# Kernel tuning notes

Measured on AMD Instinct MI355X. Metric: run time of the kernel, lower is better.

## Reference

```python
import jax, jax.numpy as jnp
import numpy as np

B, N, D, MAX_ATOMS, K = 1024, 50000, 256, 200, 8


def setup_inputs() -> dict:
    key = jax.random.key(0)
    k1, k2, k3, k4 = jax.random.split(key, 4)
    return {
        "query_embedding": jax.random.normal(k1, (B, D), dtype=jnp.float32),
        "memory_embeddings": jax.random.normal(k2, (N, D), dtype=jnp.float32),
        "memory_som_masks": jax.random.uniform(k3, (N, MAX_ATOMS), dtype=jnp.float32),
        "W": jax.random.normal(k4, (D, D), dtype=jnp.float32) / jnp.sqrt(jnp.float32(D)),
        "b": jnp.zeros((D,), dtype=jnp.float32),
        "k": K,
    }


def _to_poincare(x, W, b):
    # Linear + Tanh, then rescale into the Poincare ball (radius <= 0.95)
    h = jnp.tanh(x @ W + b)
    norm = jnp.linalg.norm(h, axis=-1, keepdims=True)
    scale = jnp.where(norm > 0.95, 0.95 / norm, jnp.ones_like(norm))
    return h * scale


def _hyperbolic_distance(x, y):
    # ||x_i - y_j||^2 via expansion (same math as broadcasted diff, no [B,N,D] blowup)
    x_sq = jnp.sum(x * x, axis=-1, keepdims=True)            # [B,1]
    y_sq = jnp.sum(y * y, axis=-1)[None, :]                   # [1,N]
    diff_sq = jnp.maximum(x_sq + y_sq - 2.0 * (x @ y.T), 0.0)  # [B,N]
    denom = (1.0 - x_sq) * (1.0 - y_sq)
    arg = 1.0 + 2.0 * diff_sq / (denom + 1e-8)
    return jnp.arccosh(jnp.maximum(arg, 1.0 + 1e-6))


def reference(query_embedding, memory_embeddings, memory_som_masks, W, b, k):
    query_hyp = _to_poincare(query_embedding, W, b)
    memory_hyp = _to_poincare(memory_embeddings, W, b)
    dists = _hyperbolic_distance(query_hyp, memory_hyp)       # [B,N]
    # smallest-k distances
    neg_top, top_idx = jax.lax.top_k(-dists, k)               # [B,k]
    top_dists = -neg_top
    weights = jax.nn.softmax(-top_dists, axis=-1)             # [B,k]
    som_hints = memory_som_masks[top_idx]                     # [B,k,MAX_ATOMS]
    return weights, som_hints
```

## Files before the change

### kernel.cpp

```cpp
#include <hip/hip_runtime.h>
#include <hip/hip_bf16.h>
#include <math.h>
#include <float.h>

#define B_Q   1024
#define N_M   50000
#define DIM   256
#define ATOMS 200
#define KSEL  8
#define NCHUNK 40
#define CHUNK  1250
#define MT    128
#define NMT   10
#define CPC   8
#define NC    (NCHUNK * CPC)
#define T16   16
#define TROWS 64
#define APX   264

typedef __attribute__((ext_vector_type(8))) short bf16x8;
typedef __attribute__((ext_vector_type(4))) float f32x4;

static __device__ inline unsigned short f2bf(float f) {
  __hip_bfloat16 h = __float2bfloat16(f);
  return *reinterpret_cast<unsigned short*>(&h);
}

static __device__ inline void split3(float x, unsigned short& s1,
                                     unsigned short& s2, unsigned short& s3) {
  __hip_bfloat16 b1 = __float2bfloat16(x);
  float f1 = __bfloat162float(b1);
  float r1 = x - f1;
  __hip_bfloat16 b2 = __float2bfloat16(r1);
  float f2 = __bfloat162float(b2);
  __hip_bfloat16 b3 = __float2bfloat16(r1 - f2);
  s1 = *reinterpret_cast<unsigned short*>(&b1);
  s2 = *reinterpret_cast<unsigned short*>(&b2);
  s3 = *reinterpret_cast<unsigned short*>(&b3);
}

static __device__ inline void split3t(float x, unsigned short& s1,
                                      unsigned short& s2, unsigned short& s3) {
  const unsigned u = __float_as_uint(x);
  s1 = (unsigned short)(u >> 16);
  const float f1 = __uint_as_float(u & 0xffff0000u);
  const float r1 = x - f1;
  const unsigned v = __float_as_uint(r1);
  s2 = (unsigned short)(v >> 16);
  const float f2 = __uint_as_float(v & 0xffff0000u);
  const float r2 = r1 - f2;
  s3 = (unsigned short)(__float_as_uint(r2) >> 16);
}

static __device__ inline float tanh32(float z) {
  float tz = fabsf(z) * 2.885390082f;
  tz = fminf(tz, 120.f);
  const float E = __builtin_amdgcn_exp2f(tz);
  const float T = 1.f - 2.f / (E + 1.f);
  return (z >= 0.f) ? T : -T;
}

__global__ __launch_bounds__(256) void wsplit_kernel(
    const float* __restrict__ W,
    unsigned short* __restrict__ Wt1, unsigned short* __restrict__ Wt2,
    unsigned short* __restrict__ Wt3)
{
  const int n = blockIdx.x;
  const int k = threadIdx.x;
  unsigned short s1, s2, s3;
  split3(W[(size_t)k * DIM + n], s1, s2, s3);
  Wt1[(size_t)n * DIM + k] = s1;
  Wt2[(size_t)n * DIM + k] = s2;
  Wt3[(size_t)n * DIM + k] = s3;
}

__global__ __launch_bounds__(1024) void transform_kernel(
    const float* __restrict__ X, int nrows,
    const unsigned short* __restrict__ Wt1, const unsigned short* __restrict__ Wt2,
    const unsigned short* __restrict__ Wt3, const float* __restrict__ bvec,
    float* __restrict__ H, unsigned short* __restrict__ Hb,
    float2* __restrict__ aux)
{
  __shared__ __align__(16) unsigned short X1s[TROWS * APX];
  __shared__ __align__(16) unsigned short X2s[TROWS * APX];
  __shared__ __align__(16) unsigned short X3s[TROWS * APX];
  __shared__ float red[16][TROWS];
  __shared__ float sArr[TROWS];

  const int t    = threadIdx.x;
  const int lane = t & 63;
  const int wave = t >> 6;
  const int row0 = blockIdx.x * TROWS;

  {
    const int r  = t >> 4;
    const int c0 = (t & 15) * 16;
    int gr = row0 + r; if (gr >= nrows) gr = nrows - 1;
    const float4* src = (const float4*)(X + (size_t)gr * DIM + c0);
    bf16x8 p1[2], p2[2], p3[2];
#pragma unroll
    for (int half = 0; half < 2; ++half) {
#pragma unroll
      for (int v = 0; v < 2; ++v) {
        const float4 x4 = src[half * 2 + v];
        const float xv[4] = {x4.x, x4.y, x4.z, x4.w};
#pragma unroll
        for (int i = 0; i < 4; ++i) {
          unsigned short s1, s2, s3;
          split3t(xv[i], s1, s2, s3);
          p1[half][v * 4 + i] = (short)s1;
          p2[half][v * 4 + i] = (short)s2;
          p3[half][v * 4 + i] = (short)s3;
        }
      }
      *(bf16x8*)(X1s + r * APX + c0 + half * 8) = p1[half];
      *(bf16x8*)(X2s + r * APX + c0 + half * 8) = p2[half];
      *(bf16x8*)(X3s + r * APX + c0 + half * 8) = p3[half];
    }
  }
  __syncthreads();

  const int lx   = lane & 15;
  const int quad = lane >> 4;
  const int n0   = wave * 16;

  f32x4 acc[4];
#pragma unroll
  for (int ms = 0; ms < 4; ++ms) { acc[ms][0] = 0.f; acc[ms][1] = 0.f; acc[ms][2] = 0.f; acc[ms][3] = 0.f; }

  const size_t brow = (size_t)(n0 + lx) * DIM + quad * 8;
  bf16x8 b1c = *(const bf16x8*)(Wt1 + brow);
  bf16x8 b2c = *(const bf16x8*)(Wt2 + brow);
  bf16x8 b3c = *(const bf16x8*)(Wt3 + brow);

#pragma unroll
  for (int ks = 0; ks < 8; ++ks) {
    bf16x8 b1n, b2n, b3n;
    if (ks < 7) {
      const size_t nb = brow + (ks + 1) * 32;
      b1n = *(const bf16x8*)(Wt1 + nb);
      b2n = *(const bf16x8*)(Wt2 + nb);
      b3n = *(const bf16x8*)(Wt3 + nb);
    }
    const int ko = ks * 32 + quad * 8;
#pragma unroll
    for (int ms = 0; ms < 4; ++ms) {
      const int ar = (ms * 16 + lx) * APX + ko;
      const bf16x8 a1 = *(const bf16x8*)(X1s + ar);
      const bf16x8 a2 = *(const bf16x8*)(X2s + ar);
      const bf16x8 a3 = *(const bf16x8*)(X3s + ar);
      acc[ms] = __builtin_amdgcn_mfma_f32_16x16x32_bf16(a1, b1c, acc[ms], 0, 0, 0);
      acc[ms] = __builtin_amdgcn_mfma_f32_16x16x32_bf16(a1, b2c, acc[ms], 0, 0, 0);
      acc[ms] = __builtin_amdgcn_mfma_f32_16x16x32_bf16(a2, b1c, acc[ms], 0, 0, 0);
      acc[ms] = __builtin_amdgcn_mfma_f32_16x16x32_bf16(a1, b3c, acc[ms], 0, 0, 0);
      acc[ms] = __builtin_amdgcn_mfma_f32_16x16x32_bf16(a2, b2c, acc[ms], 0, 0, 0);
      acc[ms] = __builtin_amdgcn_mfma_f32_16x16x32_bf16(a3, b1c, acc[ms], 0, 0, 0);
    }
    b1c = b1n; b2c = b2n; b3c = b3n;
  }

  const float bb = bvec[n0 + lx];
  float h[4][4];
#pragma unroll
  for (int ms = 0; ms < 4; ++ms)
#pragma unroll
    for (int r = 0; r < 4; ++r)
      h[ms][r] = tanh32(acc[ms][r] + bb);

  float p[4][4];
#pragma unroll
  for (int ms = 0; ms < 4; ++ms)
#pragma unroll
    for (int r = 0; r < 4; ++r) p[ms][r] = h[ms][r] * h[ms][r];
#pragma unroll
  for (int off = 1; off < 16; off <<= 1)
#pragma unroll
    for (int ms = 0; ms < 4; ++ms)
#pragma unroll
      for (int r = 0; r < 4; ++r) p[ms][r] += __shfl_xor(p[ms][r], off);
  if (lx == 0)
#pragma unroll
    for (int ms = 0; ms < 4; ++ms)
#pragma unroll
      for (int r = 0; r < 4; ++r) red[wave][ms * 16 + quad * 4 + r] = p[ms][r];
  __syncthreads();

  if (t < TROWS) {
    float nsq = 0.f;
#pragma unroll
    for (int w = 0; w < 16; ++w) nsq += red[w][t];
    const float nrm = sqrtf(nsq);
    sArr[t] = (nrm > 0.95f) ? (0.95f / nrm) : 1.f;
  }
  __syncthreads();

  float u[4][4];
#pragma unroll
  for (int ms = 0; ms < 4; ++ms)
#pragma unroll
    for (int r = 0; r < 4; ++r) {
      const float sc = sArr[ms * 16 + quad * 4 + r];
      u[ms][r] = h[ms][r] * sc;
      p[ms][r] = u[ms][r] * u[ms][r];
    }
#pragma unroll
  for (int off = 1; off < 16; off <<= 1)
#pragma unroll
    for (int ms = 0; ms < 4; ++ms)
#pragma unroll
      for (int r = 0; r < 4; ++r) p[ms][r] += __shfl_xor(p[ms][r], off);
  if (lx == 0)
#pragma unroll
    for (int ms = 0; ms < 4; ++ms)
#pragma unroll
      for (int r = 0; r < 4; ++r) red[wave][ms * 16 + quad * 4 + r] = p[ms][r];

#pragma unroll
  for (int ms = 0; ms < 4; ++ms)
#pragma unroll
    for (int r = 0; r < 4; ++r) {
      const int grow = row0 + ms * 16 + quad * 4 + r;
      if (grow < nrows) {
        H[(size_t)grow * DIM + n0 + lx]  = u[ms][r];
        Hb[(size_t)grow * DIM + n0 + lx] = f2bf(u[ms][r]);
      }
    }
  __syncthreads();
  if (t < TROWS) {
    const int grow = row0 + t;
    if (grow < nrows) {
      float ysq = 0.f;
#pragma unroll
      for (int w = 0; w < 16; ++w) ysq += red[w][t];
      aux[grow] = make_float2(ysq, 1.f / (1.f - ysq));
    }
  }
}

__global__ __launch_bounds__(256) void score_kernel(
    const unsigned short* __restrict__ Hqb, const unsigned short* __restrict__ Hmb,
    const float2* __restrict__ auxq, const float2* __restrict__ auxm,
    float* __restrict__ cand_s, int* __restrict__ cand_i)
{
  __shared__ __align__(16) unsigned short Afs[16 * 64 * 8];
  __shared__ unsigned long long wtop[4][32][CPC];

  const int t    = threadIdx.x;
  const int lane = t & 63;
  const int wave = t >> 6;
  const int q0   = blockIdx.y * 32;
  const int c    = blockIdx.x;
  const int mbase = c * CHUNK;
  const int lx   = lane & 15;
  const int quad = lane >> 4;

#pragma unroll
  for (int i = 0; i < 4; ++i) {
    const int sl = wave * 4 + i;
    const int ks = sl >> 1, qs = sl & 1;
    const bf16x8 a = *(const bf16x8*)(Hqb + (size_t)(q0 + qs * 16 + lx) * DIM + ks * 32 + quad * 8);
    *(bf16x8*)(Afs + ((size_t)sl * 64 + lane) * 8) = a;
  }
  const float xq0 = auxq[q0 +      quad * 4 + 0].x;
  const float xq1 = auxq[q0 +      quad * 4 + 1].x;
  const float xq2 = auxq[q0 +      quad * 4 + 2].x;
  const float xq3 = auxq[q0 +      quad * 4 + 3].x;
  const float xq4 = auxq[q0 + 16 + quad * 4 + 0].x;
  const float xq5 = auxq[q0 + 16 + quad * 4 + 1].x;
  const float xq6 = auxq[q0 + 16 + quad * 4 + 2].x;
  const float xq7 = auxq[q0 + 16 + quad * 4 + 3].x;
  __syncthreads();

  unsigned long long t0a=~0ULL,t0b=~0ULL,t0c=~0ULL, t1a=~0ULL,t1b=~0ULL,t1c=~0ULL;
  unsigned long long t2a=~0ULL,t2b=~0ULL,t2c=~0ULL, t3a=~0ULL,t3b=~0ULL,t3c=~0ULL;
  unsigned long long t4a=~0ULL,t4b=~0ULL,t4c=~0ULL, t5a=~0ULL,t5b=~0ULL,t5c=~0ULL;
  unsigned long long t6a=~0ULL,t6b=~0ULL,t6c=~0ULL, t7a=~0ULL,t7b=~0ULL,t7c=~0ULL;

  const int colw = wave * 32 + lx;
  int midx = mbase + colw;

  const unsigned short* B0p = Hmb + (size_t)midx * DIM + quad * 8;
  const unsigned short* B1p = B0p + (size_t)16 * DIM;

#define KSTEP(KS, BA, BB) do {                                                        \
    const bf16x8 a0_ = *(const bf16x8*)(Afs + (((KS) * 2 + 0) * 64 + lane) * 8);      \
    const bf16x8 a1_ = *(const bf16x8*)(Afs + (((KS) * 2 + 1) * 64 + lane) * 8);      \
    acc00 = __builtin_amdgcn_mfma_f32_16x16x32_bf16(a0_, BA, acc00, 0, 0, 0);         \
    acc01 = __builtin_amdgcn_mfma_f32_16x16x32_bf16(a0_, BB, acc01, 0, 0, 0);         \
    acc10 = __builtin_amdgcn_mfma_f32_16x16x32_bf16(a1_, BA, acc10, 0, 0, 0);         \
    acc11 = __builtin_amdgcn_mfma_f32_16x16x32_bf16(a1_, BB, acc11, 0, 0, 0);         \
  } while (0)

#define SCOREU(ACC, R, YM, RO, GI, XQ, T0, T1, T2) do {                               \
    const float sv_ = fmaxf(fmaf(-2.f, (ACC)[R], (XQ) + (YM)), 0.f) * (RO);           \
    const unsigned long long pk_ =                                                     \
      (((unsigned long long)__float_as_uint(sv_)) << 32) | (unsigned int)(GI);         \
    if (pk_ < T2) {                                                                    \
      T2 = pk_;                                                                        \
      if (T2 < T1) { const unsigned long long x_ = T1; T1 = T2; T2 = x_; }             \
      if (T1 < T0) { const unsigned long long x_ = T0; T0 = T1; T1 = x_; }             \
    }                                                                                  \
  } while (0)

#define SCOREM(ACC, R, YM, RO, OK, GI, XQ, T0, T1, T2) do {                           \
    const float sv_ = fmaxf(fmaf(-2.f, (ACC)[R], (XQ) + (YM)), 0.f) * (RO);           \
    const unsigned long long pk_ =                                                     \
      (((unsigned long long)__float_as_uint(sv_)) << 32) | (unsigned int)(GI);         \
    if ((OK) && pk_ < T2) {                                                            \
      T2 = pk_;                                                                        \
      if (T2 < T1) { const unsigned long long x_ = T1; T1 = T2; T2 = x_; }             \
      if (T1 < T0) { const unsigned long long x_ = T0; T0 = T1; T1 = x_; }             \
    }                                                                                  \
  } while (0)

#define SCORE16U do {                                                                 \
    const float ym0 = aux0.x, ro0 = aux0.y;                                           \
    const float ym1 = aux1.x, ro1 = aux1.y;                                           \
    const int   gi0 = midx;                                                           \
    const int   gi1 = midx + 16;                                                      \
    SCOREU(acc00, 0, ym0, ro0, gi0, xq0, t0a, t0b, t0c);                              \
    SCOREU(acc00, 1, ym0, ro0, gi0, xq1, t1a, t1b, t1c);                              \
    SCOREU(acc00, 2, ym0, ro0, gi0, xq2, t2a, t2b, t2c);                              \
    SCOREU(acc00, 3, ym0, ro0, gi0, xq3, t3a, t3b, t3c);                              \
    SCOREU(acc01, 0, ym1, ro1, gi1, xq0, t0a, t0b, t0c);                              \
    SCOREU(acc01, 1, ym1, ro1, gi1, xq1, t1a, t1b, t1c);                              \
    SCOREU(acc01, 2, ym1, ro1, gi1, xq2, t2a, t2b, t2c);                              \
    SCOREU(acc01, 3, ym1, ro1, gi1, xq3, t3a, t3b, t3c);                              \
    SCOREU(acc10, 0, ym0, ro0, gi0, xq4, t4a, t4b, t4c);                              \
    SCOREU(acc10, 1, ym0, ro0, gi0, xq5, t5a, t5b, t5c);                              \
    SCOREU(acc10, 2, ym0, ro0, gi0, xq6, t6a, t6b, t6c);                              \
    SCOREU(acc10, 3, ym0, ro0, gi0, xq7, t7a, t7b, t7c);                              \
    SCOREU(acc11, 0, ym1, ro1, gi1, xq4, t4a, t4b, t4c);                              \
    SCOREU(acc11, 1, ym1, ro1, gi1, xq5, t5a, t5b, t5c);                              \
    SCOREU(acc11, 2, ym1, ro1, gi1, xq6, t6a, t6b, t6c);                              \
    SCOREU(acc11, 3, ym1, ro1, gi1, xq7, t7a, t7b, t7c);                              \
  } while (0)

#define SCORE16M(OK0, OK1) do {                                                       \
    const float ym0 = aux0.x, ro0 = aux0.y;                                           \
    const float ym1 = aux1.x, ro1 = aux1.y;                                           \
    const int   gi0 = midx;                                                           \
    const int   gi1 = midx + 16;                                                      \
    SCOREM(acc00, 0, ym0, ro0, OK0, gi0, xq0, t0a, t0b, t0c);                         \
    SCOREM(acc00, 1, ym0, ro0, OK0, gi0, xq1, t1a, t1b, t1c);                         \
    SCOREM(acc00, 2, ym0, ro0, OK0, gi0, xq2, t2a, t2b, t2c);                         \
    SCOREM(acc00, 3, ym0, ro0, OK0, gi0, xq3, t3a, t3b, t3c);                         \
    SCOREM(acc01, 0, ym1, ro1, OK1, gi1, xq0, t0a, t0b, t0c);                         \
    SCOREM(acc01, 1, ym1, ro1, OK1, gi1, xq1, t1a, t1b, t1c);                         \
    SCOREM(acc01, 2, ym1, ro1, OK1, gi1, xq2, t2a, t2b, t2c);                         \
    SCOREM(acc01, 3, ym1, ro1, OK1, gi1, xq3, t3a, t3b, t3c);                         \
    SCOREM(acc10, 0, ym0, ro0, OK0, gi0, xq4, t4a, t4b, t4c);                         \
    SCOREM(acc10, 1, ym0, ro0, OK0, gi0, xq5, t5a, t5b, t5c);                         \
    SCOREM(acc10, 2, ym0, ro0, OK0, gi0, xq6, t6a, t6b, t6c);                         \
    SCOREM(acc10, 3, ym0, ro0, OK0, gi0, xq7, t7a, t7b, t7c);                         \
    SCOREM(acc11, 0, ym1, ro1, OK1, gi1, xq4, t4a, t4b, t4c);                         \
    SCOREM(acc11, 1, ym1, ro1, OK1, gi1, xq5, t5a, t5b, t5c);                         \
    SCOREM(acc11, 2, ym1, ro1, OK1, gi1, xq6, t6a, t6b, t6c);                         \
    SCOREM(acc11, 3, ym1, ro1, OK1, gi1, xq7, t7a, t7b, t7c);                         \
  } while (0)

  bf16x8 xA0 = *(const bf16x8*)(B0p + 0);
  bf16x8 xA1 = *(const bf16x8*)(B0p + 32);
  bf16x8 xA2 = *(const bf16x8*)(B0p + 64);
  bf16x8 xA3 = *(const bf16x8*)(B0p + 96);
  bf16x8 xB0 = *(const bf16x8*)(B1p + 0);
  bf16x8 xB1 = *(const bf16x8*)(B1p + 32);
  bf16x8 xB2 = *(const bf16x8*)(B1p + 64);
  bf16x8 xB3 = *(const bf16x8*)(B1p + 96);

  for (int mt = 0; mt < NMT - 1; ++mt) {
    bf16x8 yA0 = *(const bf16x8*)(B0p + 128);
    bf16x8 yA1 = *(const bf16x8*)(B0p + 160);
    bf16x8 yA2 = *(const bf16x8*)(B0p + 192);
    bf16x8 yA3 = *(const bf16x8*)(B0p + 224);
    bf16x8 yB0 = *(const bf16x8*)(B1p + 128);
    bf16x8 yB1 = *(const bf16x8*)(B1p + 160);
    bf16x8 yB2 = *(const bf16x8*)(B1p + 192);
    bf16x8 yB3 = *(const bf16x8*)(B1p + 224);
    const float2 aux0 = auxm[midx];
    const float2 aux1 = auxm[midx + 16];

    f32x4 acc00 = {0.f, 0.f, 0.f, 0.f};
    f32x4 acc01 = {0.f, 0.f, 0.f, 0.f};
    f32x4 acc10 = {0.f, 0.f, 0.f, 0.f};
    f32x4 acc11 = {0.f, 0.f, 0.f, 0.f};

    KSTEP(0, xA0, xB0);
    KSTEP(1, xA1, xB1);
    KSTEP(2, xA2, xB2);
    KSTEP(3, xA3, xB3);

    B0p += (size_t)MT * DIM;
    B1p += (size_t)MT * DIM;
    xA0 = *(const bf16x8*)(B0p + 0);
    xA1 = *(const bf16x8*)(B0p + 32);
    xA2 = *(const bf16x8*)(B0p + 64);
    xA3 = *(const bf16x8*)(B0p + 96);
    xB0 = *(const bf16x8*)(B1p + 0);
    xB1 = *(const bf16x8*)(B1p + 32);
    xB2 = *(const bf16x8*)(B1p + 64);
    xB3 = *(const bf16x8*)(B1p + 96);

    KSTEP(4, yA0, yB0);
    KSTEP(5, yA1, yB1);
    KSTEP(6, yA2, yB2);
    KSTEP(7, yA3, yB3);

    SCORE16U;
    midx += MT;
  }

  {
    const int rem = CHUNK - (NMT - 1) * MT;
    const bool ok0 = colw < rem;
    const bool ok1 = colw + 16 < rem;
    bf16x8 yA0 = *(const bf16x8*)(B0p + 128);
    bf16x8 yA1 = *(const bf16x8*)(B0p + 160);
    bf16x8 yA2 = *(const bf16x8*)(B0p + 192);
    bf16x8 yA3 = *(const bf16x8*)(B0p + 224);
    bf16x8 yB0 = *(const bf16x8*)(B1p + 128);
    bf16x8 yB1 = *(const bf16x8*)(B1p + 160);
    bf16x8 yB2 = *(const bf16x8*)(B1p + 192);
    bf16x8 yB3 = *(const bf16x8*)(B1p + 224);
    const float2 aux0 = auxm[midx];
    const float2 aux1 = auxm[midx + 16];

    f32x4 acc00 = {0.f, 0.f, 0.f, 0.f};
    f32x4 acc01 = {0.f, 0.f, 0.f, 0.f};
    f32x4 acc10 = {0.f, 0.f, 0.f, 0.f};
    f32x4 acc11 = {0.f, 0.f, 0.f, 0.f};

    KSTEP(0, xA0, xB0);
    KSTEP(1, xA1, xB1);
    KSTEP(2, xA2, xB2);
    KSTEP(3, xA3, xB3);
    KSTEP(4, yA0, yB0);
    KSTEP(5, yA1, yB1);
    KSTEP(6, yA2, yB2);
    KSTEP(7, yA3, yB3);

    SCORE16M(ok0, ok1);
  }

#undef KSTEP
#undef SCOREU
#undef SCOREM
#undef SCORE16U
#undef SCORE16M

#define EXTRACT_ROW(WIDX, T0, T1, T2) do {                                            \
    unsigned long long p0 = T0, p1 = T1, p2 = T2;                                     \
    for (int rd = 0; rd < CPC; ++rd) {                                                \
      unsigned long long lm = (p0 < p1) ? p0 : p1;                                    \
      lm = (p2 < lm) ? p2 : lm;                                                       \
      unsigned long long gm = lm;                                                     \
      for (int off = 1; off < 16; off <<= 1) {                                        \
        const unsigned long long o = __shfl_xor(gm, off);                             \
        gm = (o < gm) ? o : gm;                                                       \
      }                                                                               \
      if      (p0 == gm) p0 = ~0ULL;                                                  \
      else if (p1 == gm) p1 = ~0ULL;                                                  \
      else if (p2 == gm) p2 = ~0ULL;                                                  \
      if (lx == 0) wtop[wave][WIDX][rd] = gm;                                         \
    }                                                                                 \
  } while (0)

  EXTRACT_ROW(quad * 4 + 0,      t0a, t0b, t0c);
  EXTRACT_ROW(quad * 4 + 1,      t1a, t1b, t1c);
  EXTRACT_ROW(quad * 4 + 2,      t2a, t2b, t2c);
  EXTRACT_ROW(quad * 4 + 3,      t3a, t3b, t3c);
  EXTRACT_ROW(16 + quad * 4 + 0, t4a, t4b, t4c);
  EXTRACT_ROW(16 + quad * 4 + 1, t5a, t5b, t5c);
  EXTRACT_ROW(16 + quad * 4 + 2, t6a, t6b, t6c);
  EXTRACT_ROW(16 + quad * 4 + 3, t7a, t7b, t7c);
#undef EXTRACT_ROW
  __syncthreads();

  {
    const int qr = t >> 3;
    const int sp = t & 7;
    unsigned long long v0 = wtop[0][qr][sp];
    unsigned long long v1 = wtop[1][qr][sp];
    unsigned long long v2 = wtop[2][qr][sp];
    unsigned long long v3 = wtop[3][qr][sp];
    const size_t cbase = ((size_t)(q0 + qr) * NCHUNK + c) * CPC;
    for (int rd = 0; rd < CPC; ++rd) {
      unsigned long long lm = (v0 < v1) ? v0 : v1;
      const unsigned long long l2 = (v2 < v3) ? v2 : v3;
      lm = (l2 < lm) ? l2 : lm;
      unsigned long long gm = lm;
#pragma unroll
      for (int off = 1; off < 8; off <<= 1) {
        const unsigned long long o = __shfl_xor(gm, off);
        gm = (o < gm) ? o : gm;
      }
      if      (v0 == gm) v0 = ~0ULL;
      else if (v1 == gm) v1 = ~0ULL;
      else if (v2 == gm) v2 = ~0ULL;
      else if (v3 == gm) v3 = ~0ULL;
      if (sp == 0) {
        cand_s[cbase + rd] = __uint_as_float((unsigned int)(gm >> 32));
        cand_i[cbase + rd] = (int)(unsigned int)(gm & 0xffffffffu);
      }
    }
  }
}

__global__ __launch_bounds__(256) void finalize_kernel(
    const float* __restrict__ Hq, const float* __restrict__ Hm,
    const float* __restrict__ masks,
    const float* __restrict__ cand_s, const int* __restrict__ cand_i,
    float* __restrict__ outW, float* __restrict__ outH)
{
  const int q    = blockIdx.x;
  const int t    = threadIdx.x;
  const int lane = t & 63;
  const int wave = t >> 6;

  __shared__ unsigned long long wtop[4][T16];
  __shared__ int    selIdx[T16];
  __shared__ double dArr[T16];
  __shared__ int    fin_i[KSEL];
  __shared__ double fin_d[KSEL];
  __shared__ double ew[KSEL];

  {
    const size_t base = (size_t)q * NC + (size_t)wave * (NC / 4);
    unsigned long long pk[2];
#pragma unroll
    for (int s = 0; s < 2; ++s) {
      const int c = lane + 64 * s;
      pk[s] = (c < NC / 4)
        ? ((((unsigned long long)__float_as_uint(cand_s[base + c])) << 32) | (unsigned int)cand_i[base + c])
        : ~0ULL;
    }
    for (int r = 0; r < T16; ++r) {
      unsigned long long lm = (pk[0] < pk[1]) ? pk[0] : pk[1];
      unsigned long long gm = lm;
#pragma unroll
      for (int off = 1; off < 64; off <<= 1) {
        unsigned long long o = __shfl_xor(gm, off);
        gm = (o < gm) ? o : gm;
      }
      bool done = false;
#pragma unroll
      for (int s = 0; s < 2; ++s) if (!done && pk[s] == gm) { pk[s] = ~0ULL; done = true; }
      if (lane == 0) wtop[wave][r] = gm;
    }
  }
  __syncthreads();

  if (wave == 0) {
    unsigned long long v = wtop[lane >> 4][lane & 15];
    for (int r = 0; r < T16; ++r) {
      unsigned long long gm = v;
#pragma unroll
      for (int off = 1; off < 64; off <<= 1) {
        unsigned long long o = __shfl_xor(gm, off);
        gm = (o < gm) ? o : gm;
      }
      if (v == gm) v = ~0ULL;
      if (lane == 0) selIdx[r] = (int)(unsigned int)(gm & 0xffffffffULL);
    }
  }
  __syncthreads();

  const float4 q4 = *(const float4*)(Hq + (size_t)q * DIM + 4 * lane);
  double xp_ = (double)q4.x * q4.x + (double)q4.y * q4.y + (double)q4.z * q4.z + (double)q4.w * q4.w;
#pragma unroll
  for (int off = 1; off < 64; off <<= 1) xp_ += __shfl_xor(xp_, off);
  const double xsq = xp_;

  for (int r = wave; r < T16; r += 4) {
    const int cidx = selIdx[r];
    const float4 m4 = *(const float4*)(Hm + (size_t)cidx * DIM + 4 * lane);
    double dp = (double)q4.x * m4.x + (double)q4.y * m4.y + (double)q4.z * m4.z + (double)q4.w * m4.w;
    double yp = (double)m4.x * m4.x + (double)m4.y * m4.y + (double)m4.z * m4.z + (double)m4.w * m4.w;
#pragma unroll
    for (int off = 1; off < 64; off <<= 1) { dp += __shfl_xor(dp, off); yp += __shfl_xor(yp, off); }
    if (lane == 0) {
      double diff = xsq + yp - 2.0 * dp; if (diff < 0.0) diff = 0.0;
      double den = (1.0 - xsq) * (1.0 - yp);
      double arg = 1.0 + 2.0 * diff / (den + 1e-8);
      const double lo = 1.0 + 1e-6;
      if (arg < lo) arg = lo;
      dArr[r] = log(arg + sqrt(arg * arg - 1.0));
    }
  }
  __syncthreads();

  if (t < T16) {
    const double dj = dArr[t]; const int ij = selIdx[t];
    int rank = 0;
#pragma unroll
    for (int i = 0; i < T16; ++i)
      rank += (dArr[i] < dj || (dArr[i] == dj && selIdx[i] < ij)) ? 1 : 0;
    if (rank < KSEL) { fin_d[rank] = dj; fin_i[rank] = ij; }
  }
  __syncthreads();
  if (t < KSEL) ew[t] = exp(fin_d[0] - fin_d[t]);
  __syncthreads();
  if (t < KSEL) {
    double ssum = 0.0;
#pragma unroll
    for (int i = 0; i < KSEL; ++i) ssum += ew[i];
    outW[(size_t)q * KSEL + t] = (float)(ew[t] / ssum);
  }

  const int g  = t >> 5;
  const int l0 = t & 31;
  const int row = fin_i[g];
  for (int l = l0; l < ATOMS; l += 32)
    outH[((size_t)q * KSEL + g) * ATOMS + l] = masks[(size_t)row * ATOMS + l];
}

extern "C" void kernel_launch(void* const* d_in, const int* in_sizes, int n_in,
                              void* d_out, int out_size, void* d_ws, size_t ws_size,
                              hipStream_t stream) {
  const float* Q     = (const float*)d_in[0];
  const float* M     = (const float*)d_in[1];
  const float* masks = (const float*)d_in[2];
  const float* W     = (const float*)d_in[3];
  const float* bv    = (const float*)d_in[4];

  char* w = (char*)d_ws;
  float*          Hq   = (float*)(w);
  float*          Hm   = (float*)(w + 1048576);
  unsigned short* Hqb  = (unsigned short*)(w + 52248576);
  unsigned short* Hmb  = (unsigned short*)(w + 52772864);
  float2*         auxq = (float2*)(w + 78397440);
  float2*         auxm = (float2*)(w + 78405632);
  float*          cs   = (float*)(w + 78806016);
  int*            cix  = (int*)(w + 80116736);

  unsigned short* Wt1 = (unsigned short*)(w + 78806016);
  unsigned short* Wt2 = Wt1 + DIM * DIM;
  unsigned short* Wt3 = Wt2 + DIM * DIM;

  wsplit_kernel<<<DIM, DIM, 0, stream>>>(W, Wt1, Wt2, Wt3);
  transform_kernel<<<(B_Q + TROWS - 1) / TROWS, 1024, 0, stream>>>(Q, B_Q, Wt1, Wt2, Wt3, bv, Hq, Hqb, auxq);
  transform_kernel<<<(N_M + TROWS - 1) / TROWS, 1024, 0, stream>>>(M, N_M, Wt1, Wt2, Wt3, bv, Hm, Hmb, auxm);
  score_kernel<<<dim3(NCHUNK, B_Q / 32), 256, 0, stream>>>(Hqb, Hmb, auxq, auxm, cs, cix);
  finalize_kernel<<<B_Q, 256, 0, stream>>>(Hq, Hm, masks, cs, cix,
                                           (float*)d_out, (float*)d_out + (size_t)B_Q * KSEL);
}
```

Measured before the change: 399.7 us.

## Store bf16 embeddings in MFMA fragment-tiled layout for contiguous per-lane loads

The projection kernel now writes the bf16 query and memory embeddings in a tiled order of 16-row by 32-column fragments. In this order each wave's MFMA operand load reads one contiguous 1 KB block instead of row-strided 16-byte pieces. CHUNK grows to 1280 so that chunks line up with 128-row tiles. Every chunk except the last now runs full unmasked tiles, and only the last chunk does a single masked tile. This relies on the tail reads beyond N staying inside the allocated buffers.

```diff
diff --git a/kernel.cpp b/kernel.cpp
--- a/kernel.cpp
+++ b/kernel.cpp
@@ -9,7 +9,7 @@
 #define ATOMS 200
 #define KSEL  8
 #define NCHUNK 40
-#define CHUNK  1250
+#define CHUNK  1280
 #define MT    128
 #define NMT   10
 #define CPC   8
@@ -215,14 +215,18 @@
 #pragma unroll
       for (int r = 0; r < 4; ++r) red[wave][ms * 16 + quad * 4 + r] = p[ms][r];
 
+  const int colv = n0 + lx;
+  const int ksb  = colv >> 5;
+  const int qoff = ((colv >> 3) & 3) * 128 + (colv & 7);
 #pragma unroll
   for (int ms = 0; ms < 4; ++ms)
 #pragma unroll
     for (int r = 0; r < 4; ++r) {
       const int grow = row0 + ms * 16 + quad * 4 + r;
       if (grow < nrows) {
-        H[(size_t)grow * DIM + n0 + lx]  = u[ms][r];
-        Hb[(size_t)grow * DIM + n0 + lx] = f2bf(u[ms][r]);
+        H[(size_t)grow * DIM + colv] = u[ms][r];
+        Hb[((size_t)((row0 >> 4) + ms) * 8 + ksb) * 512 + qoff + (quad * 4 + r) * 8]
+            = f2bf(u[ms][r]);
       }
     }
   __syncthreads();
@@ -258,7 +262,7 @@
   for (int i = 0; i < 4; ++i) {
     const int sl = wave * 4 + i;
     const int ks = sl >> 1, qs = sl & 1;
-    const bf16x8 a = *(const bf16x8*)(Hqb + (size_t)(q0 + qs * 16 + lx) * DIM + ks * 32 + quad * 8);
+    const bf16x8 a = *(const bf16x8*)(Hqb + ((size_t)((q0 >> 4) + qs) * 8 + ks) * 512 + (size_t)lane * 8);
     *(bf16x8*)(Afs + ((size_t)sl * 64 + lane) * 8) = a;
   }
   const float xq0 = auxq[q0 +      quad * 4 + 0].x;
@@ -279,8 +283,8 @@
   const int colw = wave * 32 + lx;
   int midx = mbase + colw;
 
-  const unsigned short* B0p = Hmb + (size_t)midx * DIM + quad * 8;
-  const unsigned short* B1p = B0p + (size_t)16 * DIM;
+  const unsigned short* Bp = Hmb + (size_t)((mbase >> 4) + wave * 2) * 4096 + (size_t)lane * 8;
+#define LD(OFS) (*(const bf16x8*)(Bp + (OFS)))
 
 #define KSTEP(KS, BA, BB) do {                                                        \
     const bf16x8 a0_ = *(const bf16x8*)(Afs + (((KS) * 2 + 0) * 64 + lane) * 8);      \
@@ -359,69 +363,70 @@
     SCOREM(acc11, 3, ym1, ro1, OK1, gi1, xq7, t7a, t7b, t7c);                         \
   } while (0)
 
-  bf16x8 xA0 = *(const bf16x8*)(B0p + 0);
-  bf16x8 xA1 = *(const bf16x8*)(B0p + 32);
-  bf16x8 xA2 = *(const bf16x8*)(B0p + 64);
-  bf16x8 xA3 = *(const bf16x8*)(B0p + 96);
-  bf16x8 xB0 = *(const bf16x8*)(B1p + 0);
-  bf16x8 xB1 = *(const bf16x8*)(B1p + 32);
-  bf16x8 xB2 = *(const bf16x8*)(B1p + 64);
-  bf16x8 xB3 = *(const bf16x8*)(B1p + 96);
-
-  for (int mt = 0; mt < NMT - 1; ++mt) {
-    bf16x8 yA0 = *(const bf16x8*)(B0p + 128);
-    bf16x8 yA1 = *(const bf16x8*)(B0p + 160);
-    bf16x8 yA2 = *(const bf16x8*)(B0p + 192);
-    bf16x8 yA3 = *(const bf16x8*)(B0p + 224);
-    bf16x8 yB0 = *(const bf16x8*)(B1p + 128);
-    bf16x8 yB1 = *(const bf16x8*)(B1p + 160);
-    bf16x8 yB2 = *(const bf16x8*)(B1p + 192);
-    bf16x8 yB3 = *(const bf16x8*)(B1p + 224);
-    const float2 aux0 = auxm[midx];
-    const float2 aux1 = auxm[midx + 16];
-
-    f32x4 acc00 = {0.f, 0.f, 0.f, 0.f};
-    f32x4 acc01 = {0.f, 0.f, 0.f, 0.f};
-    f32x4 acc10 = {0.f, 0.f, 0.f, 0.f};
-    f32x4 acc11 = {0.f, 0.f, 0.f, 0.f};
-
-    KSTEP(0, xA0, xB0);
-    KSTEP(1, xA1, xB1);
-    KSTEP(2, xA2, xB2);
-    KSTEP(3, xA3, xB3);
-
-    B0p += (size_t)MT * DIM;
-    B1p += (size_t)MT * DIM;
-    xA0 = *(const bf16x8*)(B0p + 0);
-    xA1 = *(const bf16x8*)(B0p + 32);
-    xA2 = *(const bf16x8*)(B0p + 64);
-    xA3 = *(const bf16x8*)(B0p + 96);
-    xB0 = *(const bf16x8*)(B1p + 0);
-    xB1 = *(const bf16x8*)(B1p + 32);
-    xB2 = *(const bf16x8*)(B1p + 64);
-    xB3 = *(const bf16x8*)(B1p + 96);
-
-    KSTEP(4, yA0, yB0);
-    KSTEP(5, yA1, yB1);
-    KSTEP(6, yA2, yB2);
-    KSTEP(7, yA3, yB3);
-
-    SCORE16U;
-    midx += MT;
-  }
-
-  {
-    const int rem = CHUNK - (NMT - 1) * MT;
-    const bool ok0 = colw < rem;
-    const bool ok1 = colw + 16 < rem;
-    bf16x8 yA0 = *(const bf16x8*)(B0p + 128);
-    bf16x8 yA1 = *(const bf16x8*)(B0p + 160);
-    bf16x8 yA2 = *(const bf16x8*)(B0p + 192);
-    bf16x8 yA3 = *(const bf16x8*)(B0p + 224);
-    bf16x8 yB0 = *(const bf16x8*)(B1p + 128);
-    bf16x8 yB1 = *(const bf16x8*)(B1p + 160);
-    bf16x8 yB2 = *(const bf16x8*)(B1p + 192);
-    bf16x8 yB3 = *(const bf16x8*)(B1p + 224);
+  if (c != NCHUNK - 1) {
+    bf16x8 xA0 = LD(0),    xA1 = LD(512),  xA2 = LD(1024), xA3 = LD(1536);
+    bf16x8 xB0 = LD(4096), xB1 = LD(4608), xB2 = LD(5120), xB3 = LD(5632);
+
+    for (int mt = 0; mt < NMT - 1; ++mt) {
+      bf16x8 yA0 = LD(2048), yA1 = LD(2560), yA2 = LD(3072), yA3 = LD(3584);
+      bf16x8 yB0 = LD(6144), yB1 = LD(6656), yB2 = LD(7168), yB3 = LD(7680);
+      const float2 aux0 = auxm[midx];
+      const float2 aux1 = auxm[midx + 16];
+
+      f32x4 acc00 = {0.f, 0.f, 0.f, 0.f};
+      f32x4 acc01 = {0.f, 0.f, 0.f, 0.f};
+      f32x4 acc10 = {0.f, 0.f, 0.f, 0.f};
+      f32x4 acc11 = {0.f, 0.f, 0.f, 0.f};
+
+      KSTEP(0, xA0, xB0);
+      KSTEP(1, xA1, xB1);
+      KSTEP(2, xA2, xB2);
+      KSTEP(3, xA3, xB3);
+
+      Bp += 8 * 4096;
+      xA0 = LD(0);    xA1 = LD(512);  xA2 = LD(1024); xA3 = LD(1536);
+      xB0 = LD(4096); xB1 = LD(4608); xB2 = LD(5120); xB3 = LD(5632);
+
+      KSTEP(4, yA0, yB0);
+      KSTEP(5, yA1, yB1);
+      KSTEP(6, yA2, yB2);
+      KSTEP(7, yA3, yB3);
+
+      SCORE16U;
+      midx += MT;
+    }
+
+    {
+      bf16x8 yA0 = LD(2048), yA1 = LD(2560), yA2 = LD(3072), yA3 = LD(3584);
+      bf16x8 yB0 = LD(6144), yB1 = LD(6656), yB2 = LD(7168), yB3 = LD(7680);
+      const float2 aux0 = auxm[midx];
+      const float2 aux1 = auxm[midx + 16];
+
+      f32x4 acc00 = {0.f, 0.f, 0.f, 0.f};
+      f32x4 acc01 = {0.f, 0.f, 0.f, 0.f};
+      f32x4 acc10 = {0.f, 0.f, 0.f, 0.f};
+      f32x4 acc11 = {0.f, 0.f, 0.f, 0.f};
+
+      KSTEP(0, xA0, xB0);
+      KSTEP(1, xA1, xB1);
+      KSTEP(2, xA2, xB2);
+      KSTEP(3, xA3, xB3);
+      KSTEP(4, yA0, yB0);
+      KSTEP(5, yA1, yB1);
+      KSTEP(6, yA2, yB2);
+      KSTEP(7, yA3, yB3);
+
+      SCORE16U;
+    }
+  } else {
+    const int vrem = N_M - mbase;
+    const bool ok0 = colw < vrem;
+    const bool ok1 = colw + 16 < vrem;
+
+    bf16x8 xA0 = LD(0),    xA1 = LD(512),  xA2 = LD(1024), xA3 = LD(1536);
+    bf16x8 xB0 = LD(4096), xB1 = LD(4608), xB2 = LD(5120), xB3 = LD(5632);
+    bf16x8 yA0 = LD(2048), yA1 = LD(2560), yA2 = LD(3072), yA3 = LD(3584);
+    bf16x8 yB0 = LD(6144), yB1 = LD(6656), yB2 = LD(7168), yB3 = LD(7680);
     const float2 aux0 = auxm[midx];
     const float2 aux1 = auxm[midx + 16];
 
@@ -442,6 +447,7 @@
     SCORE16M(ok0, ok1);
   }
 
+#undef LD
 #undef KSTEP
 #undef SCOREU
 #undef SCOREM
```

Measured after the change: 360.0 us. 1.11x faster.
